# Kernel optimization log

Hardware: AMD Instinct MI355X
Metric: run time of the kernel (lower is better)

## Reference

```python
import jax, jax.numpy as jnp
import numpy as np

HEADS = 16

def setup_inputs() -> dict:
    key = jax.random.key(0)
    ks = jax.random.split(key, 5)
    dim = 1024
    x = jax.random.normal(ks[0], (2, 2048, dim), dtype=jnp.float32)
    scale = 1.0 / np.sqrt(dim)
    Wq = jax.random.normal(ks[1], (dim, dim), dtype=jnp.float32) * scale
    Wk = jax.random.normal(ks[2], (dim, dim), dtype=jnp.float32) * scale
    Wv = jax.random.normal(ks[3], (dim, dim), dtype=jnp.float32) * scale
    Wo = jax.random.normal(ks[4], (dim, dim), dtype=jnp.float32) * scale
    return {"x": x, "Wq": Wq, "Wk": Wk, "Wv": Wv, "Wo": Wo}

def reference(x, Wq, Wk, Wv, Wo):
    b, n, dim = x.shape
    h = HEADS
    d = dim // h
    # projections: torch Linear y = x @ W.T (W is [out,in])
    def split_heads(t):
        return t.reshape(b, n, h, d).transpose(0, 2, 1, 3)  # b h n d
    q = split_heads(x @ Wq.T)
    k = split_heads(x @ Wk.T)
    v = split_heads(x @ Wv.T)
    scale = jnp.asarray(d, x.dtype) ** -0.5
    dots = jnp.einsum('bhid,bhjd->bhij', q, k) * scale
    # causal mask: positions j > i masked (triu with diagonal 1 since i == j)
    i_idx = jnp.arange(n)[:, None]
    j_idx = jnp.arange(n)[None, :]
    mask_value = -jnp.finfo(dots.dtype).max
    dots = jnp.where(j_idx > i_idx, mask_value, dots)
    attn = jax.nn.softmax(dots, axis=-1)  # dropout p=0 (eval) is identity
    out = jnp.einsum('bhij,bhjd->bhid', attn, v)
    out = out.transpose(0, 2, 1, 3).reshape(b, n, dim)
    return out @ Wo.T
```

## Files before the change

kernel.cpp:

```cpp
#include <hip/hip_runtime.h>
#include <hip/hip_bf16.h>

#define BATCH 2
#define SEQ   2048
#define DIM   1024
#define HEADS 16
#define DIMH  64
#define BK    32
#define LOG2E 1.44269504088896340736f
#define SM_SHIFT 16.0f

typedef __attribute__((ext_vector_type(8))) short short8;
typedef __attribute__((ext_vector_type(4))) short short4v;
typedef __attribute__((ext_vector_type(4))) float floatx4;

static __device__ __forceinline__ void gload_lds16(const void* g, void* l) {
    __builtin_amdgcn_global_load_lds(
        (const __attribute__((address_space(1))) void*)g,
        (__attribute__((address_space(3))) void*)l, 16, 0, 0);
}

static __device__ __forceinline__ unsigned pkbf(float a, float b) {
    __hip_bfloat16 ta = __float2bfloat16(a);
    __hip_bfloat16 tb = __float2bfloat16(b);
    return (unsigned)*reinterpret_cast<unsigned short*>(&ta) |
           ((unsigned)*reinterpret_cast<unsigned short*>(&tb) << 16);
}

__global__ __launch_bounds__(256) void conv_bf16(
    const float* __restrict__ x,  const float* __restrict__ Wq,
    const float* __restrict__ Wk, const float* __restrict__ Wv,
    __hip_bfloat16* __restrict__ dst)
{
    const size_t NX = (size_t)BATCH * SEQ * DIM;
    const size_t NW = (size_t)DIM * DIM;
    size_t i = ((size_t)blockIdx.x * 256 + threadIdx.x) * 4;
    if (i >= NX + 3 * NW) return;
    const float* src; size_t off;
    if (i < NX) { src = x; off = i; }
    else {
        size_t j = i - NX;
        int w = (int)(j >> 20);
        src = (w == 0) ? Wq : (w == 1) ? Wk : Wv;
        off = j & (NW - 1);
    }
    floatx4 f = *reinterpret_cast<const floatx4*>(src + off);
    short4v o;
    #pragma unroll
    for (int e = 0; e < 4; ++e) {
        __hip_bfloat16 t = __float2bfloat16(f[e]);
        o[e] = *reinterpret_cast<short*>(&t);
    }
    *reinterpret_cast<short4v*>((short*)dst + i) = o;
}

__global__ __launch_bounds__(256) void conv_wo(
    const float* __restrict__ W, __hip_bfloat16* __restrict__ dst)
{
    size_t i = ((size_t)blockIdx.x * 256 + threadIdx.x) * 4;
    floatx4 f = *reinterpret_cast<const floatx4*>(W + i);
    short4v o;
    #pragma unroll
    for (int e = 0; e < 4; ++e) {
        __hip_bfloat16 t = __float2bfloat16(f[e]);
        o[e] = *reinterpret_cast<short*>(&t);
    }
    *reinterpret_cast<short4v*>((short*)dst + i) = o;
}

__global__ __launch_bounds__(256) void gemm_qkv(
    const __hip_bfloat16* __restrict__ xbf,
    const __hip_bfloat16* __restrict__ wbf,
    __hip_bfloat16* __restrict__ qkv)
{
    __shared__ __align__(16) short As[128 * BK];
    __shared__ __align__(16) short Bs[128 * BK];

    const int tid  = threadIdx.x;
    const int wv   = tid >> 6;
    const int lane = tid & 63;
    const int quad = lane >> 4;
    const int l16  = lane & 15;
    const int wm   = wv >> 1, wn = wv & 1;
    const int m0   = blockIdx.x * 128;
    const int n0   = blockIdx.y * 128;
    const int z    = n0 >> 10;
    __hip_bfloat16* out = qkv + (size_t)z * (BATCH * SEQ * DIM);

    const int srow = tid >> 2;
    const int scol = (tid & 3) * 8;

    floatx4 acc[4][4] = {};

    for (int k0 = 0; k0 < DIM; k0 += BK) {
        __syncthreads();
        #pragma unroll
        for (int i = 0; i < 2; ++i) {
            const __hip_bfloat16* ga = xbf + (size_t)(m0 + srow + i * 64) * DIM + k0 + scol;
            const __hip_bfloat16* gb = wbf + (size_t)(n0 + srow + i * 64) * DIM + k0 + scol;
            gload_lds16(ga, (char*)As + i * 4096 + wv * 1024);
            gload_lds16(gb, (char*)Bs + i * 4096 + wv * 1024);
        }
        __syncthreads();

        short8 af[4], bf[4];
        #pragma unroll
        for (int mt = 0; mt < 4; ++mt)
            af[mt] = *reinterpret_cast<const short8*>(&As[(wm * 64 + mt * 16 + l16) * 32 + quad * 8]);
        #pragma unroll
        for (int nt = 0; nt < 4; ++nt)
            bf[nt] = *reinterpret_cast<const short8*>(&Bs[(wn * 64 + nt * 16 + l16) * 32 + quad * 8]);
        #pragma unroll
        for (int mt = 0; mt < 4; ++mt)
            #pragma unroll
            for (int nt = 0; nt < 4; ++nt)
                acc[mt][nt] = __builtin_amdgcn_mfma_f32_16x16x32_bf16(
                    af[mt], bf[nt], acc[mt][nt], 0, 0, 0);
    }

    const float esc = (z == 0) ? (0.125f * LOG2E) : 1.0f;
    #pragma unroll
    for (int mt = 0; mt < 4; ++mt) {
        #pragma unroll
        for (int nt = 0; nt < 4; ++nt) {
            const int n  = n0 + wn * 64 + nt * 16 + l16;
            const int hh = (n >> 6) & 15, dv = n & 63;
            #pragma unroll
            for (int r = 0; r < 4; ++r) {
                const int m  = m0 + wm * 64 + mt * 16 + quad * 4 + r;
                const int bb = m >> 11, nn = m & (SEQ - 1);
                const float v = acc[mt][nt][r] * esc;
                if (z < 2)
                    out[((size_t)(bb * HEADS + hh) * SEQ + nn) * DIMH + dv] = __float2bfloat16(v);
                else
                    out[((size_t)(bb * HEADS + hh) * DIMH + dv) * SEQ + nn] = __float2bfloat16(v);
            }
        }
    }
}

__global__ __launch_bounds__(256) void gemm_out(
    const __hip_bfloat16* __restrict__ A,
    const __hip_bfloat16* __restrict__ W,
    float* __restrict__ C)
{
    __shared__ __align__(16) short As[128 * BK];
    __shared__ __align__(16) short Bs[128 * BK];

    const int tid  = threadIdx.x;
    const int wv   = tid >> 6;
    const int lane = tid & 63;
    const int quad = lane >> 4;
    const int l16  = lane & 15;
    const int wm   = wv >> 1, wn = wv & 1;
    const int m0   = blockIdx.x * 128;
    const int n0   = blockIdx.y * 128;

    const int srow = tid >> 2;
    const int scol = (tid & 3) * 8;

    floatx4 acc[4][4] = {};

    for (int k0 = 0; k0 < DIM; k0 += BK) {
        __syncthreads();
        #pragma unroll
        for (int i = 0; i < 2; ++i) {
            const __hip_bfloat16* ga = A + (size_t)(m0 + srow + i * 64) * DIM + k0 + scol;
            const __hip_bfloat16* gb = W + (size_t)(n0 + srow + i * 64) * DIM + k0 + scol;
            gload_lds16(ga, (char*)As + i * 4096 + wv * 1024);
            gload_lds16(gb, (char*)Bs + i * 4096 + wv * 1024);
        }
        __syncthreads();

        short8 af[4], bf[4];
        #pragma unroll
        for (int mt = 0; mt < 4; ++mt)
            af[mt] = *reinterpret_cast<const short8*>(&As[(wm * 64 + mt * 16 + l16) * 32 + quad * 8]);
        #pragma unroll
        for (int nt = 0; nt < 4; ++nt)
            bf[nt] = *reinterpret_cast<const short8*>(&Bs[(wn * 64 + nt * 16 + l16) * 32 + quad * 8]);
        #pragma unroll
        for (int mt = 0; mt < 4; ++mt)
            #pragma unroll
            for (int nt = 0; nt < 4; ++nt)
                acc[mt][nt] = __builtin_amdgcn_mfma_f32_16x16x32_bf16(
                    af[mt], bf[nt], acc[mt][nt], 0, 0, 0);
    }

    #pragma unroll
    for (int mt = 0; mt < 4; ++mt)
        #pragma unroll
        for (int nt = 0; nt < 4; ++nt) {
            const int n = n0 + wn * 64 + nt * 16 + l16;
            #pragma unroll
            for (int r = 0; r < 4; ++r) {
                const int m = m0 + wm * 64 + mt * 16 + quad * 4 + r;
                C[(size_t)m * DIM + n] = acc[mt][nt][r];
            }
        }
}

__global__ __launch_bounds__(128) void attn_causal(
    const __hip_bfloat16* __restrict__ qkv,
    __hip_bfloat16* __restrict__ omat)
{
    __shared__ __align__(16) short kt[64 * 64];
    __shared__ __align__(16) short vt[64 * 64];
    __shared__ __align__(16) short pt[2][16 * 72];

    const int id    = blockIdx.x;
    const int combo = id & 31;
    const int p     = id >> 5;
    const int b     = combo >> 4;
    const int h     = combo & 15;
    const int tA = p, tB = 63 - p;
    const int nA = (tA + 2) >> 1;
    const int nB = (tB + 2) >> 1;
    const int total = nA + nB;

    const size_t hoff = (size_t)(b * HEADS + h) * SEQ * DIMH;
    const size_t one  = (size_t)BATCH * SEQ * DIM;
    const __hip_bfloat16* qb  = qkv + hoff;
    const __hip_bfloat16* kb  = qkv + one + hoff;
    const __hip_bfloat16* vtg = qkv + 2 * one + hoff;

    const int tid  = threadIdx.x;
    const int wv   = tid >> 6;
    const int lane = tid & 63;
    const int quad = lane >> 4;
    const int l16  = lane & 15;
    const int xr   = l16 & 7;

    const short8 kones = {0x3F80, 0x3F80, 0x3F80, 0x3F80,
                          0x3F80, 0x3F80, 0x3F80, 0x3F80};

    int q16 = tA * 32 + wv * 16;
    short8 aq0 = *reinterpret_cast<const short8*>(qb + (size_t)(q16 + l16) * DIMH + quad * 8);
    short8 aq1 = *reinterpret_cast<const short8*>(qb + (size_t)(q16 + l16) * DIMH + 32 + quad * 8);
    floatx4 oacc[4] = {};
    floatx4 lsum = {};

    short8 kreg[4], vreg[4];
    #pragma unroll
    for (int i = 0; i < 4; ++i) {
        const int c = tid + 128 * i;
        const int row = c >> 3, jc = c & 7;
        kreg[i] = *reinterpret_cast<const short8*>(kb + (size_t)row * DIMH + jc * 8);
        vreg[i] = *reinterpret_cast<const short8*>(vtg + (size_t)row * SEQ + jc * 8);
    }

    for (int s = 0; s < total; ++s) {
        const bool lastA = (s == nA - 1);
        const int j0 = ((s < nA) ? s : s - nA) * 64;

        __syncthreads();
        #pragma unroll
        for (int i = 0; i < 4; ++i) {
            const int c = tid + 128 * i;
            const int row = c >> 3, jc = c & 7;
            const int off = row * 64 + ((jc ^ (row & 7)) * 8);
            *reinterpret_cast<short8*>(&kt[off]) = kreg[i];
            *reinterpret_cast<short8*>(&vt[off]) = vreg[i];
        }
        __syncthreads();

        if (s + 1 < total) {
            const int s2 = s + 1;
            const int j1 = ((s2 < nA) ? s2 : s2 - nA) * 64;
            #pragma unroll
            for (int i = 0; i < 4; ++i) {
                const int c = tid + 128 * i;
                const int row = c >> 3, jc = c & 7;
                kreg[i] = *reinterpret_cast<const short8*>(kb + (size_t)(j1 + row) * DIMH + jc * 8);
                vreg[i] = *reinterpret_cast<const short8*>(vtg + (size_t)row * SEQ + j1 + jc * 8);
            }
        }

        floatx4 st[4];
        #pragma unroll
        for (int t = 0; t < 4; ++t) {
            const int rw = t * 16 + l16;
            short8 a0 = *reinterpret_cast<const short8*>(&kt[rw * 64 + (quad ^ xr) * 8]);
            short8 a1 = *reinterpret_cast<const short8*>(&kt[rw * 64 + ((quad + 4) ^ xr) * 8]);
            floatx4 zz = {};
            zz    = __builtin_amdgcn_mfma_f32_16x16x32_bf16(a0, aq0, zz, 0, 0, 0);
            st[t] = __builtin_amdgcn_mfma_f32_16x16x32_bf16(a1, aq1, zz, 0, 0, 0);
        }

        if (j0 + 63 > q16) {
            const int qg = q16 + l16;
            #pragma unroll
            for (int t = 0; t < 4; ++t)
                #pragma unroll
                for (int r = 0; r < 4; ++r) {
                    const int jg = j0 + t * 16 + quad * 4 + r;
                    if (jg > qg) st[t][r] = -3.0e38f;
                }
        }

        #pragma unroll
        for (int t = 0; t < 4; ++t)
            #pragma unroll
            for (int r = 0; r < 4; ++r)
                st[t][r] = __builtin_amdgcn_exp2f(st[t][r] - SM_SHIFT);

        #pragma unroll
        for (int t = 0; t < 4; ++t) {
            *reinterpret_cast<unsigned*>(&pt[wv][l16 * 72 + t * 16 + quad * 4]) =
                pkbf(st[t][0], st[t][1]);
            *reinterpret_cast<unsigned*>(&pt[wv][l16 * 72 + t * 16 + quad * 4 + 2]) =
                pkbf(st[t][2], st[t][3]);
        }
        short8 p0 = *reinterpret_cast<const short8*>(&pt[wv][l16 * 72 + quad * 8]);
        short8 p1 = *reinterpret_cast<const short8*>(&pt[wv][l16 * 72 + 32 + quad * 8]);

        lsum = __builtin_amdgcn_mfma_f32_16x16x32_bf16(kones, p0, lsum, 0, 0, 0);
        lsum = __builtin_amdgcn_mfma_f32_16x16x32_bf16(kones, p1, lsum, 0, 0, 0);

        #pragma unroll
        for (int dt = 0; dt < 4; ++dt) {
            const int rw = dt * 16 + l16;
            short8 v0 = *reinterpret_cast<const short8*>(&vt[rw * 64 + (quad ^ xr) * 8]);
            short8 v1 = *reinterpret_cast<const short8*>(&vt[rw * 64 + ((quad + 4) ^ xr) * 8]);
            oacc[dt] = __builtin_amdgcn_mfma_f32_16x16x32_bf16(v0, p0, oacc[dt], 0, 0, 0);
            oacc[dt] = __builtin_amdgcn_mfma_f32_16x16x32_bf16(v1, p1, oacc[dt], 0, 0, 0);
        }

        if (lastA || s == total - 1) {
            const float rl = 1.0f / lsum[0];
            #pragma unroll
            for (int dt = 0; dt < 4; ++dt)
                #pragma unroll
                for (int r = 0; r < 4; ++r) {
                    const int dv = dt * 16 + quad * 4 + r;
                    omat[(size_t)(b * SEQ + q16 + l16) * DIM + h * DIMH + dv] =
                        __float2bfloat16(oacc[dt][r] * rl);
                }
            if (lastA) {
                q16 = tB * 32 + wv * 16;
                aq0 = *reinterpret_cast<const short8*>(qb + (size_t)(q16 + l16) * DIMH + quad * 8);
                aq1 = *reinterpret_cast<const short8*>(qb + (size_t)(q16 + l16) * DIMH + 32 + quad * 8);
                #pragma unroll
                for (int dt = 0; dt < 4; ++dt)
                    #pragma unroll
                    for (int r = 0; r < 4; ++r) oacc[dt][r] = 0.f;
                #pragma unroll
                for (int r = 0; r < 4; ++r) lsum[r] = 0.f;
            }
        }
    }
}


extern "C" void kernel_launch(void* const* d_in, const int* in_sizes, int n_in,
                              void* d_out, int out_size, void* d_ws, size_t ws_size,
                              hipStream_t stream) {
    const float* x  = (const float*)d_in[0];
    const float* Wq = (const float*)d_in[1];
    const float* Wk = (const float*)d_in[2];
    const float* Wv = (const float*)d_in[3];
    const float* Wo = (const float*)d_in[4];

    __hip_bfloat16* qkv  = (__hip_bfloat16*)d_ws;
    __hip_bfloat16* omat = qkv + (size_t)3 * BATCH * SEQ * DIM;
    __hip_bfloat16* wobf = (__hip_bfloat16*)d_ws;

    __hip_bfloat16* xbf = (__hip_bfloat16*)d_out;
    __hip_bfloat16* wbf = xbf + (size_t)BATCH * SEQ * DIM;

    conv_bf16 <<<7168, 256, 0, stream>>>(x, Wq, Wk, Wv, xbf);
    gemm_qkv  <<<dim3((BATCH * SEQ) / 128, (3 * DIM) / 128), 256, 0, stream>>>(xbf, wbf, qkv);
    attn_causal<<<dim3(1024), 128, 0, stream>>>(qkv, omat);
    conv_wo   <<<1024, 256, 0, stream>>>(Wo, wobf);
    gemm_out  <<<dim3((BATCH * SEQ) / 128, DIM / 128),       256, 0, stream>>>(omat, wobf, (float*)d_out);
}
```

Measured before the change: 194.6 us.

## Merge conversions, widen GEMM K tiles with swizzle, drop P LDS round-trip in attention

Fuses the Wo conversion into the single input-conversion kernel, removing one launch. Both GEMMs move to BK=64 with XOR-swizzled LDS, and the output GEMM uses 64-row tiles. It reads attention output straight from the head-major buffer, because attention now writes its result in place over Q instead of to a separate matrix. Attention uses the 16x16x16 MFMA so the exponentiated P stays in registers without the LDS round-trip, and P packing now truncates instead of rounding to bf16. The costs are slightly lower precision and extra in-place aliasing assumptions on the workspace.

```diff
diff --git a/kernel.cpp b/kernel.cpp
--- a/kernel.cpp
+++ b/kernel.cpp
@@ -6,13 +6,18 @@
 #define DIM   1024
 #define HEADS 16
 #define DIMH  64
-#define BK    32
 #define LOG2E 1.44269504088896340736f
 #define SM_SHIFT 16.0f
 
 typedef __attribute__((ext_vector_type(8))) short short8;
 typedef __attribute__((ext_vector_type(4))) short short4v;
 typedef __attribute__((ext_vector_type(4))) float floatx4;
+
+#if defined(__has_builtin)
+#if __has_builtin(__builtin_amdgcn_mfma_f32_16x16x16bf16_1k)
+#define HAVE_MFMA16 1
+#endif
+#endif
 
 static __device__ __forceinline__ void gload_lds16(const void* g, void* l) {
     __builtin_amdgcn_global_load_lds(
@@ -20,52 +25,39 @@
         (__attribute__((address_space(3))) void*)l, 16, 0, 0);
 }
 
-static __device__ __forceinline__ unsigned pkbf(float a, float b) {
-    __hip_bfloat16 ta = __float2bfloat16(a);
-    __hip_bfloat16 tb = __float2bfloat16(b);
-    return (unsigned)*reinterpret_cast<unsigned short*>(&ta) |
-           ((unsigned)*reinterpret_cast<unsigned short*>(&tb) << 16);
-}
-
-__global__ __launch_bounds__(256) void conv_bf16(
+static __device__ __forceinline__ unsigned pk_trunc(float a, float b) {
+    return (__float_as_uint(b) & 0xffff0000u) | (__float_as_uint(a) >> 16);
+}
+
+__global__ __launch_bounds__(256) void conv_all(
     const float* __restrict__ x,  const float* __restrict__ Wq,
     const float* __restrict__ Wk, const float* __restrict__ Wv,
-    __hip_bfloat16* __restrict__ dst)
+    const float* __restrict__ Wo,
+    __hip_bfloat16* __restrict__ dst, __hip_bfloat16* __restrict__ dwo)
 {
     const size_t NX = (size_t)BATCH * SEQ * DIM;
     const size_t NW = (size_t)DIM * DIM;
     size_t i = ((size_t)blockIdx.x * 256 + threadIdx.x) * 4;
-    if (i >= NX + 3 * NW) return;
-    const float* src; size_t off;
-    if (i < NX) { src = x; off = i; }
-    else {
+    if (i >= NX + 4 * NW) return;
+    const float* src; __hip_bfloat16* d;
+    if (i < NX) { src = x + i; d = dst + i; }
+    else if (i < NX + 3 * NW) {
         size_t j = i - NX;
         int w = (int)(j >> 20);
-        src = (w == 0) ? Wq : (w == 1) ? Wk : Wv;
-        off = j & (NW - 1);
-    }
-    floatx4 f = *reinterpret_cast<const floatx4*>(src + off);
+        src = ((w == 0) ? Wq : (w == 1) ? Wk : Wv) + (j & (NW - 1));
+        d = dst + i;
+    } else {
+        size_t off = i - (NX + 3 * NW);
+        src = Wo + off; d = dwo + off;
+    }
+    floatx4 f = *reinterpret_cast<const floatx4*>(src);
     short4v o;
     #pragma unroll
     for (int e = 0; e < 4; ++e) {
         __hip_bfloat16 t = __float2bfloat16(f[e]);
         o[e] = *reinterpret_cast<short*>(&t);
     }
-    *reinterpret_cast<short4v*>((short*)dst + i) = o;
-}
-
-__global__ __launch_bounds__(256) void conv_wo(
-    const float* __restrict__ W, __hip_bfloat16* __restrict__ dst)
-{
-    size_t i = ((size_t)blockIdx.x * 256 + threadIdx.x) * 4;
-    floatx4 f = *reinterpret_cast<const floatx4*>(W + i);
-    short4v o;
-    #pragma unroll
-    for (int e = 0; e < 4; ++e) {
-        __hip_bfloat16 t = __float2bfloat16(f[e]);
-        o[e] = *reinterpret_cast<short*>(&t);
-    }
-    *reinterpret_cast<short4v*>((short*)dst + i) = o;
+    *reinterpret_cast<short4v*>(d) = o;
 }
 
 __global__ __launch_bounds__(256) void gemm_qkv(
@@ -73,49 +65,59 @@
     const __hip_bfloat16* __restrict__ wbf,
     __hip_bfloat16* __restrict__ qkv)
 {
-    __shared__ __align__(16) short As[128 * BK];
-    __shared__ __align__(16) short Bs[128 * BK];
+    __shared__ __align__(16) short As[128 * 64];
+    __shared__ __align__(16) short Bs[128 * 64];
 
     const int tid  = threadIdx.x;
     const int wv   = tid >> 6;
     const int lane = tid & 63;
     const int quad = lane >> 4;
     const int l16  = lane & 15;
+    const int xr   = l16 & 7;
     const int wm   = wv >> 1, wn = wv & 1;
     const int m0   = blockIdx.x * 128;
     const int n0   = blockIdx.y * 128;
     const int z    = n0 >> 10;
     __hip_bfloat16* out = qkv + (size_t)z * (BATCH * SEQ * DIM);
 
-    const int srow = tid >> 2;
-    const int scol = (tid & 3) * 8;
+    const int srow = tid >> 3;
+    const int sjc  = tid & 7;
 
     floatx4 acc[4][4] = {};
 
-    for (int k0 = 0; k0 < DIM; k0 += BK) {
-        __syncthreads();
-        #pragma unroll
-        for (int i = 0; i < 2; ++i) {
-            const __hip_bfloat16* ga = xbf + (size_t)(m0 + srow + i * 64) * DIM + k0 + scol;
-            const __hip_bfloat16* gb = wbf + (size_t)(n0 + srow + i * 64) * DIM + k0 + scol;
-            gload_lds16(ga, (char*)As + i * 4096 + wv * 1024);
-            gload_lds16(gb, (char*)Bs + i * 4096 + wv * 1024);
-        }
-        __syncthreads();
-
-        short8 af[4], bf[4];
-        #pragma unroll
-        for (int mt = 0; mt < 4; ++mt)
-            af[mt] = *reinterpret_cast<const short8*>(&As[(wm * 64 + mt * 16 + l16) * 32 + quad * 8]);
-        #pragma unroll
-        for (int nt = 0; nt < 4; ++nt)
-            bf[nt] = *reinterpret_cast<const short8*>(&Bs[(wn * 64 + nt * 16 + l16) * 32 + quad * 8]);
-        #pragma unroll
-        for (int mt = 0; mt < 4; ++mt)
+    for (int k0 = 0; k0 < DIM; k0 += 64) {
+        __syncthreads();
+        #pragma unroll
+        for (int i = 0; i < 4; ++i) {
+            const int row = srow + i * 32;
+            const int sg  = sjc ^ (row & 7);
+            gload_lds16(xbf + (size_t)(m0 + row) * DIM + k0 + sg * 8,
+                        (char*)As + i * 4096 + wv * 1024);
+            gload_lds16(wbf + (size_t)(n0 + row) * DIM + k0 + sg * 8,
+                        (char*)Bs + i * 4096 + wv * 1024);
+        }
+        __syncthreads();
+
+        short8 af[2][4], bf_[2][4];
+        #pragma unroll
+        for (int kk = 0; kk < 2; ++kk) {
+            #pragma unroll
+            for (int mt = 0; mt < 4; ++mt)
+                af[kk][mt] = *reinterpret_cast<const short8*>(
+                    &As[(wm * 64 + mt * 16 + l16) * 64 + ((kk * 4 + quad) ^ xr) * 8]);
             #pragma unroll
             for (int nt = 0; nt < 4; ++nt)
-                acc[mt][nt] = __builtin_amdgcn_mfma_f32_16x16x32_bf16(
-                    af[mt], bf[nt], acc[mt][nt], 0, 0, 0);
+                bf_[kk][nt] = *reinterpret_cast<const short8*>(
+                    &Bs[(wn * 64 + nt * 16 + l16) * 64 + ((kk * 4 + quad) ^ xr) * 8]);
+        }
+        #pragma unroll
+        for (int kk = 0; kk < 2; ++kk)
+            #pragma unroll
+            for (int mt = 0; mt < 4; ++mt)
+                #pragma unroll
+                for (int nt = 0; nt < 4; ++nt)
+                    acc[mt][nt] = __builtin_amdgcn_mfma_f32_16x16x32_bf16(
+                        af[kk][mt], bf_[kk][nt], acc[mt][nt], 0, 0, 0);
     }
 
     const float esc = (z == 0) ? (0.125f * LOG2E) : 1.0f;
@@ -140,73 +142,92 @@
 }
 
 __global__ __launch_bounds__(256) void gemm_out(
-    const __hip_bfloat16* __restrict__ A,
+    const __hip_bfloat16* __restrict__ qhs,
     const __hip_bfloat16* __restrict__ W,
     float* __restrict__ C)
 {
-    __shared__ __align__(16) short As[128 * BK];
-    __shared__ __align__(16) short Bs[128 * BK];
+    __shared__ __align__(16) short As[64 * 64];
+    __shared__ __align__(16) short Bs[128 * 64];
 
     const int tid  = threadIdx.x;
     const int wv   = tid >> 6;
     const int lane = tid & 63;
     const int quad = lane >> 4;
     const int l16  = lane & 15;
+    const int xr   = l16 & 7;
     const int wm   = wv >> 1, wn = wv & 1;
-    const int m0   = blockIdx.x * 128;
+    const int m0   = blockIdx.x * 64;
     const int n0   = blockIdx.y * 128;
 
-    const int srow = tid >> 2;
-    const int scol = (tid & 3) * 8;
-
-    floatx4 acc[4][4] = {};
-
-    for (int k0 = 0; k0 < DIM; k0 += BK) {
+    const int srow = tid >> 3;
+    const int sjc  = tid & 7;
+
+    floatx4 acc[2][4] = {};
+
+    for (int k0 = 0; k0 < DIM; k0 += 64) {
+        const int h = k0 >> 6;
         __syncthreads();
         #pragma unroll
         for (int i = 0; i < 2; ++i) {
-            const __hip_bfloat16* ga = A + (size_t)(m0 + srow + i * 64) * DIM + k0 + scol;
-            const __hip_bfloat16* gb = W + (size_t)(n0 + srow + i * 64) * DIM + k0 + scol;
-            gload_lds16(ga, (char*)As + i * 4096 + wv * 1024);
-            gload_lds16(gb, (char*)Bs + i * 4096 + wv * 1024);
-        }
-        __syncthreads();
-
-        short8 af[4], bf[4];
-        #pragma unroll
-        for (int mt = 0; mt < 4; ++mt)
-            af[mt] = *reinterpret_cast<const short8*>(&As[(wm * 64 + mt * 16 + l16) * 32 + quad * 8]);
-        #pragma unroll
-        for (int nt = 0; nt < 4; ++nt)
-            bf[nt] = *reinterpret_cast<const short8*>(&Bs[(wn * 64 + nt * 16 + l16) * 32 + quad * 8]);
-        #pragma unroll
-        for (int mt = 0; mt < 4; ++mt)
+            const int row = srow + i * 32;
+            const int sg  = sjc ^ (row & 7);
+            const int m   = m0 + row;
+            const int bb  = m >> 11, nn = m & (SEQ - 1);
+            gload_lds16(qhs + ((size_t)(bb * HEADS + h) * SEQ + nn) * DIMH + sg * 8,
+                        (char*)As + i * 4096 + wv * 1024);
+        }
+        #pragma unroll
+        for (int i = 0; i < 4; ++i) {
+            const int row = srow + i * 32;
+            const int sg  = sjc ^ (row & 7);
+            gload_lds16(W + (size_t)(n0 + row) * DIM + k0 + sg * 8,
+                        (char*)Bs + i * 4096 + wv * 1024);
+        }
+        __syncthreads();
+
+        short8 af[2][2], bf_[2][4];
+        #pragma unroll
+        for (int kk = 0; kk < 2; ++kk) {
+            #pragma unroll
+            for (int mt = 0; mt < 2; ++mt)
+                af[kk][mt] = *reinterpret_cast<const short8*>(
+                    &As[(wm * 32 + mt * 16 + l16) * 64 + ((kk * 4 + quad) ^ xr) * 8]);
             #pragma unroll
             for (int nt = 0; nt < 4; ++nt)
-                acc[mt][nt] = __builtin_amdgcn_mfma_f32_16x16x32_bf16(
-                    af[mt], bf[nt], acc[mt][nt], 0, 0, 0);
+                bf_[kk][nt] = *reinterpret_cast<const short8*>(
+                    &Bs[(wn * 64 + nt * 16 + l16) * 64 + ((kk * 4 + quad) ^ xr) * 8]);
+        }
+        #pragma unroll
+        for (int kk = 0; kk < 2; ++kk)
+            #pragma unroll
+            for (int mt = 0; mt < 2; ++mt)
+                #pragma unroll
+                for (int nt = 0; nt < 4; ++nt)
+                    acc[mt][nt] = __builtin_amdgcn_mfma_f32_16x16x32_bf16(
+                        af[kk][mt], bf_[kk][nt], acc[mt][nt], 0, 0, 0);
     }
 
     #pragma unroll
-    for (int mt = 0; mt < 4; ++mt)
+    for (int mt = 0; mt < 2; ++mt)
         #pragma unroll
         for (int nt = 0; nt < 4; ++nt) {
             const int n = n0 + wn * 64 + nt * 16 + l16;
             #pragma unroll
             for (int r = 0; r < 4; ++r) {
-                const int m = m0 + wm * 64 + mt * 16 + quad * 4 + r;
+                const int m = m0 + wm * 32 + mt * 16 + quad * 4 + r;
                 C[(size_t)m * DIM + n] = acc[mt][nt][r];
             }
         }
 }
 
 __global__ __launch_bounds__(128) void attn_causal(
-    const __hip_bfloat16* __restrict__ qkv,
-    __hip_bfloat16* __restrict__ omat)
+    __hip_bfloat16* __restrict__ qkv)
 {
     __shared__ __align__(16) short kt[64 * 64];
     __shared__ __align__(16) short vt[64 * 64];
+#if !defined(HAVE_MFMA16)
     __shared__ __align__(16) short pt[2][16 * 72];
+#endif
 
     const int id    = blockIdx.x;
     const int combo = id & 31;
@@ -220,7 +241,7 @@
 
     const size_t hoff = (size_t)(b * HEADS + h) * SEQ * DIMH;
     const size_t one  = (size_t)BATCH * SEQ * DIM;
-    const __hip_bfloat16* qb  = qkv + hoff;
+    __hip_bfloat16* qb        = qkv + hoff;
     const __hip_bfloat16* kb  = qkv + one + hoff;
     const __hip_bfloat16* vtg = qkv + 2 * one + hoff;
 
@@ -231,14 +252,21 @@
     const int l16  = lane & 15;
     const int xr   = l16 & 7;
 
-    const short8 kones = {0x3F80, 0x3F80, 0x3F80, 0x3F80,
-                          0x3F80, 0x3F80, 0x3F80, 0x3F80};
-
     int q16 = tA * 32 + wv * 16;
     short8 aq0 = *reinterpret_cast<const short8*>(qb + (size_t)(q16 + l16) * DIMH + quad * 8);
     short8 aq1 = *reinterpret_cast<const short8*>(qb + (size_t)(q16 + l16) * DIMH + 32 + quad * 8);
     floatx4 oacc[4] = {};
     floatx4 lsum = {};
+
+    const int srow = tid >> 3;
+    const int sch  = (tid & 7) ^ (srow & 7);
+
+#if defined(HAVE_MFMA16)
+    const short4v kone4 = {0x3F80, 0x3F80, 0x3F80, 0x3F80};
+#else
+    const short8 kone8 = {0x3F80, 0x3F80, 0x3F80, 0x3F80,
+                          0x3F80, 0x3F80, 0x3F80, 0x3F80};
+#endif
 
     short8 kreg[4], vreg[4];
     #pragma unroll
@@ -304,19 +332,48 @@
             for (int r = 0; r < 4; ++r)
                 st[t][r] = __builtin_amdgcn_exp2f(st[t][r] - SM_SHIFT);
 
+#if defined(HAVE_MFMA16)
+        short4v pa[4];
+        #pragma unroll
+        for (int t = 0; t < 4; ++t) {
+            unsigned u2[2] = { pk_trunc(st[t][0], st[t][1]),
+                               pk_trunc(st[t][2], st[t][3]) };
+            pa[t] = *reinterpret_cast<short4v*>(u2);
+        }
+        #pragma unroll
+        for (int t = 0; t < 4; ++t)
+            lsum = __builtin_amdgcn_mfma_f32_16x16x16bf16_1k(pa[t], kone4, lsum, 0, 0, 0);
+        #pragma unroll
+        for (int dt = 0; dt < 4; ++dt) {
+            const int row = dt * 16 + l16;
+            #pragma unroll
+            for (int t = 0; t < 4; ++t) {
+                short4v bv = *reinterpret_cast<const short4v*>(
+                    &vt[row * 64 + (((t * 2 + (quad >> 1)) ^ xr) * 8) + (quad & 1) * 4]);
+                oacc[dt] = __builtin_amdgcn_mfma_f32_16x16x16bf16_1k(pa[t], bv, oacc[dt], 0, 0, 0);
+            }
+        }
+        if (lastA || s == total - 1) {
+            #pragma unroll
+            for (int r = 0; r < 4; ++r) {
+                const float rl = 1.0f / lsum[r];
+                #pragma unroll
+                for (int dt = 0; dt < 4; ++dt)
+                    qb[(size_t)(q16 + quad * 4 + r) * DIMH + dt * 16 + l16] =
+                        __float2bfloat16(oacc[dt][r] * rl);
+            }
+#else
         #pragma unroll
         for (int t = 0; t < 4; ++t) {
             *reinterpret_cast<unsigned*>(&pt[wv][l16 * 72 + t * 16 + quad * 4]) =
-                pkbf(st[t][0], st[t][1]);
+                pk_trunc(st[t][0], st[t][1]);
             *reinterpret_cast<unsigned*>(&pt[wv][l16 * 72 + t * 16 + quad * 4 + 2]) =
-                pkbf(st[t][2], st[t][3]);
+                pk_trunc(st[t][2], st[t][3]);
         }
         short8 p0 = *reinterpret_cast<const short8*>(&pt[wv][l16 * 72 + quad * 8]);
         short8 p1 = *reinterpret_cast<const short8*>(&pt[wv][l16 * 72 + 32 + quad * 8]);
-
-        lsum = __builtin_amdgcn_mfma_f32_16x16x32_bf16(kones, p0, lsum, 0, 0, 0);
-        lsum = __builtin_amdgcn_mfma_f32_16x16x32_bf16(kones, p1, lsum, 0, 0, 0);
-
+        lsum = __builtin_amdgcn_mfma_f32_16x16x32_bf16(kone8, p0, lsum, 0, 0, 0);
+        lsum = __builtin_amdgcn_mfma_f32_16x16x32_bf16(kone8, p1, lsum, 0, 0, 0);
         #pragma unroll
         for (int dt = 0; dt < 4; ++dt) {
             const int rw = dt * 16 + l16;
@@ -325,17 +382,15 @@
             oacc[dt] = __builtin_amdgcn_mfma_f32_16x16x32_bf16(v0, p0, oacc[dt], 0, 0, 0);
             oacc[dt] = __builtin_amdgcn_mfma_f32_16x16x32_bf16(v1, p1, oacc[dt], 0, 0, 0);
         }
-
         if (lastA || s == total - 1) {
             const float rl = 1.0f / lsum[0];
             #pragma unroll
             for (int dt = 0; dt < 4; ++dt)
                 #pragma unroll
-                for (int r = 0; r < 4; ++r) {
-                    const int dv = dt * 16 + quad * 4 + r;
-                    omat[(size_t)(b * SEQ + q16 + l16) * DIM + h * DIMH + dv] =
+                for (int r = 0; r < 4; ++r)
+                    qb[(size_t)(q16 + l16) * DIMH + dt * 16 + quad * 4 + r] =
                         __float2bfloat16(oacc[dt][r] * rl);
-                }
+#endif
             if (lastA) {
                 q16 = tB * 32 + wv * 16;
                 aq0 = *reinterpret_cast<const short8*>(qb + (size_t)(q16 + l16) * DIMH + quad * 8);
@@ -362,15 +417,13 @@
     const float* Wo = (const float*)d_in[4];
 
     __hip_bfloat16* qkv  = (__hip_bfloat16*)d_ws;
-    __hip_bfloat16* omat = qkv + (size_t)3 * BATCH * SEQ * DIM;
-    __hip_bfloat16* wobf = (__hip_bfloat16*)d_ws;
+    __hip_bfloat16* wobf = (__hip_bfloat16*)((char*)d_ws + (size_t)24 * 1024 * 1024);
 
     __hip_bfloat16* xbf = (__hip_bfloat16*)d_out;
     __hip_bfloat16* wbf = xbf + (size_t)BATCH * SEQ * DIM;
 
-    conv_bf16 <<<7168, 256, 0, stream>>>(x, Wq, Wk, Wv, xbf);
+    conv_all  <<<8192, 256, 0, stream>>>(x, Wq, Wk, Wv, Wo, xbf, wobf);
     gemm_qkv  <<<dim3((BATCH * SEQ) / 128, (3 * DIM) / 128), 256, 0, stream>>>(xbf, wbf, qkv);
-    attn_causal<<<dim3(1024), 128, 0, stream>>>(qkv, omat);
-    conv_wo   <<<1024, 256, 0, stream>>>(Wo, wobf);
-    gemm_out  <<<dim3((BATCH * SEQ) / 128, DIM / 128),       256, 0, stream>>>(omat, wobf, (float*)d_out);
-}
+    attn_causal<<<dim3(1024), 128, 0, stream>>>(qkv);
+    gemm_out  <<<dim3((BATCH * SEQ) / 64, DIM / 128), 256, 0, stream>>>(qkv, wobf, (float*)d_out);
+}
```

After: 201.5 us. +3.5%, slower.
